# Kernel tuning notes

Measured on AMD Instinct MI355X. Metric: run time of the kernel, lower is better.

Reference implementation:

```python
import jax, jax.numpy as jnp
import numpy as np

NUM_HEADS = 16
THETA = 10000.0


def _rope(x, pos, theta):
    # x: [b, h, s, d_k] with d_k even; rotate interleaved pairs (even, odd)
    d = x.shape[-1]
    inv_freq = theta ** (-jnp.arange(0, d, 2, dtype=jnp.float32) / d)  # [d/2]
    ang = pos.astype(jnp.float32)[:, None] * inv_freq                  # [s, d/2]
    cos = jnp.cos(ang)[None, None]                                     # [1,1,s,d/2]
    sin = jnp.sin(ang)[None, None]
    x1 = x[..., 0::2]
    x2 = x[..., 1::2]
    r1 = x1 * cos - x2 * sin
    r2 = x1 * sin + x2 * cos
    return jnp.stack([r1, r2], axis=-1).reshape(x.shape)


def setup_inputs() -> dict:
    key = jax.random.key(0)
    ks = jax.random.split(key, 5)
    B, S, D = 2, 2048, 1024
    x = jax.random.normal(ks[0], (B, S, D), dtype=jnp.float32)
    scale = 0.02
    Wq = jax.random.normal(ks[1], (D, D), dtype=jnp.float32) * scale
    Wk = jax.random.normal(ks[2], (D, D), dtype=jnp.float32) * scale
    Wv = jax.random.normal(ks[3], (D, D), dtype=jnp.float32) * scale
    Wo = jax.random.normal(ks[4], (D, D), dtype=jnp.float32) * scale
    return {"x": x, "Wq": Wq, "Wk": Wk, "Wv": Wv, "Wo": Wo}


def reference(x, Wq, Wk, Wv, Wo):
    B, S, D = x.shape
    H = NUM_HEADS
    dk = D // H
    # QKV projections (bias-free Linear: y = x @ W^T, W is [out, in])
    q = (x @ Wq.T).reshape(B, S, H, dk).transpose(0, 2, 1, 3)  # [b,h,s,dk]
    k = (x @ Wk.T).reshape(B, S, H, dk).transpose(0, 2, 1, 3)
    v = (x @ Wv.T).reshape(B, S, H, dk).transpose(0, 2, 1, 3)
    pos = jnp.arange(S)
    q = _rope(q, pos, THETA)
    k = _rope(k, pos, THETA)
    # naive masked SDPA, causal mask
    scores = jnp.einsum('bhqd,bhkd->bhqk', q, k) / (dk ** 0.5)
    causal = jnp.tril(jnp.ones((S, S), dtype=bool))
    scores = jnp.where(causal, scores, -jnp.inf)
    attn = jax.nn.softmax(scores, axis=-1)
    out = jnp.einsum('bhqk,bhkd->bhqd', attn, v)
    out = out.transpose(0, 2, 1, 3).reshape(B, S, D)
    return out @ Wo.T
```

## Files before the change

### kernel.cpp

```cpp
#include <hip/hip_runtime.h>
#include <hip/hip_bf16.h>
#include <stdint.h>

typedef __bf16 bf16;
typedef __bf16 bf16x8 __attribute__((ext_vector_type(8)));
typedef float f32x4 __attribute__((ext_vector_type(4)));
typedef float f32x16 __attribute__((ext_vector_type(16)));

#define B_ 2
#define S_ 2048
#define D_ 1024
#define H_ 16
#define DK 64
#define M_ 4096

__device__ __forceinline__ void gload_lds16(const void* g, void* l) {
  __builtin_amdgcn_global_load_lds(
      (const __attribute__((address_space(1))) uint32_t*)(uintptr_t)g,
      (__attribute__((address_space(3))) uint32_t*)(uintptr_t)l, 16, 0, 0);
}

__device__ __forceinline__ uint32_t pkbf(float a, float b) {
  union { uint32_t u; struct { bf16 x, y; } s; } r;
  r.s.x = (bf16)a; r.s.y = (bf16)b;
  return r.u;
}

struct alignas(8) B4s { bf16 a, b, c, d; };

__global__ __launch_bounds__(256) void cvt_all_kernel(
    const float* __restrict__ x, const float* __restrict__ wq, const float* __restrict__ wk,
    const float* __restrict__ wv, const float* __restrict__ wo,
    bf16* __restrict__ xb, bf16* __restrict__ wqb, bf16* __restrict__ wkb,
    bf16* __restrict__ wvb, bf16* __restrict__ wob) {
  int i = blockIdx.x * 256 + threadIdx.x;
  const float* src;
  bf16* dst;
  int off;
  if (i < 1048576) { src = x; dst = xb; off = i; }
  else if (i < 1310720) { src = wq; dst = wqb; off = i - 1048576; }
  else if (i < 1572864) { src = wk; dst = wkb; off = i - 1310720; }
  else if (i < 1835008) { src = wv; dst = wvb; off = i - 1572864; }
  else { src = wo; dst = wob; off = i - 1835008; }
  float4 v = reinterpret_cast<const float4*>(src)[off];
  B4s o{(bf16)v.x, (bf16)v.y, (bf16)v.z, (bf16)v.w};
  reinterpret_cast<B4s*>(dst)[off] = o;
}

template <int MODE>
__global__ __launch_bounds__(256, 3) void gemm_kernel(
    const bf16* __restrict__ A,
    const bf16* __restrict__ W0, const bf16* __restrict__ W1, const bf16* __restrict__ W2,
    bf16* __restrict__ q_out, bf16* __restrict__ k_out, bf16* __restrict__ v_out,
    float* __restrict__ c_out) {
  constexpr int BK = 64;
  constexpr int BM = (MODE == 0) ? 128 : 64;
  constexpr int AM = (MODE == 0) ? 2 : 1;
  constexpr int NT = (MODE == 0) ? 24 : 8;
  constexpr int PERX = (MODE == 0) ? 96 : 64;
  __shared__ bf16 Alds[BM * BK];
  __shared__ bf16 Blds[128 * BK];
  const int tid = threadIdx.x;
  const int w = tid >> 6, l = tid & 63;
  const int l31 = l & 31, hh = l >> 5;
  const int lin = (blockIdx.x & 7) * PERX + (blockIdx.x >> 3);
  const int m0 = (lin / NT) * BM;
  const int nt = lin % NT;
  const bf16* W;
  int n0;
  const int rt = (MODE == 0) ? (nt >> 3) : 0;
  if (MODE == 0) {
    W = rt == 0 ? W0 : (rt == 1 ? W1 : W2);
    n0 = (nt & 7) * 128;
  } else {
    W = W0;
    n0 = nt * 128;
  }
  const int K = 1024;
  const int wm = (MODE == 0) ? (w >> 1) * 64 : (w & 1) * 32;
  const int wn = (MODE == 0) ? (w & 1) * 64 : (w >> 1) * 64;
  const int srow = w * 8 + (l >> 3);
  const int scol = ((l & 7) * 8) ^ (((l >> 3) & 7) * 8);
  const int swz = (l & 7) * 8;
  f32x16 acc[AM][2] = {};
  for (int k0 = 0; k0 < K; k0 += BK) {
    const bf16* Ab = A + (size_t)m0 * K + k0;
    const bf16* Bb = W + (size_t)n0 * K + k0;
#pragma unroll
    for (int c = 0; c < BM / 32; ++c)
      gload_lds16(Ab + (size_t)(c * 32 + srow) * K + scol, Alds + (c * 32 + w * 8) * BK);
#pragma unroll
    for (int c = 0; c < 4; ++c)
      gload_lds16(Bb + (size_t)(c * 32 + srow) * K + scol, Blds + (c * 32 + w * 8) * BK);
    __syncthreads();
    bf16x8 af[AM][4], bfr[2][4];
#pragma unroll
    for (int am = 0; am < AM; ++am)
#pragma unroll
      for (int t = 0; t < 4; ++t)
        af[am][t] = *reinterpret_cast<const bf16x8*>(
            Alds + (wm + am * 32 + l31) * BK + ((t * 16 + hh * 8) ^ swz));
#pragma unroll
    for (int bn = 0; bn < 2; ++bn)
#pragma unroll
      for (int t = 0; t < 4; ++t)
        bfr[bn][t] = *reinterpret_cast<const bf16x8*>(
            Blds + (wn + bn * 32 + l31) * BK + ((t * 16 + hh * 8) ^ swz));
#pragma unroll
    for (int t = 0; t < 4; ++t)
#pragma unroll
      for (int am = 0; am < AM; ++am)
#pragma unroll
        for (int bn = 0; bn < 2; ++bn)
          acc[am][bn] = __builtin_amdgcn_mfma_f32_32x32x16_bf16(af[am][t], bfr[bn][t],
                                                               acc[am][bn], 0, 0, 0);
    __syncthreads();
  }
#pragma unroll
  for (int am = 0; am < AM; ++am)
#pragma unroll
    for (int bn = 0; bn < 2; ++bn)
#pragma unroll
      for (int r = 0; r < 16; ++r) {
        int m = m0 + wm + am * 32 + (r & 3) + 8 * (r >> 2) + 4 * hh;
        int n = n0 + wn + bn * 32 + l31;
        float v = acc[am][bn][r];
        if (MODE == 0) {
          bf16* dst = rt == 0 ? q_out : (rt == 1 ? k_out : v_out);
          int h = n >> 6, d = n & 63;
          int b = m >> 11, s = m & 2047;
          dst[(((size_t)b * H_ + h) * S_ + s) * DK + d] = (bf16)v;
        } else {
          c_out[(size_t)m * D_ + n] = v;
        }
      }
}

__global__ __launch_bounds__(256) void rope_kernel(bf16* __restrict__ Q, bf16* __restrict__ K) {
  const int NG = 32 * 2048 * 8;
  int idx = blockIdx.x * 256 + threadIdx.x;
  bf16* X = Q;
  float sc = 0.18033688f;
  if (idx >= NG) { X = K; idx -= NG; sc = 1.0f; }
  int g = idx & 7;
  int s = (idx >> 3) & 2047;
  int bh = idx >> 14;
  size_t off = ((size_t)bh * S_ + s) * DK + g * 8;
  bf16x8 v = *reinterpret_cast<const bf16x8*>(X + off);
  bf16x8 o;
  const float c0 = -0.4152410118609203f;
  float fs = (float)s;
#pragma unroll
  for (int p = 0; p < 4; ++p) {
    int i = g * 4 + p;
    float ang = fs * exp2f((float)i * c0);
    float sn = __sinf(ang), cs = __cosf(ang);
    float x1 = (float)v[2 * p], x2 = (float)v[2 * p + 1];
    o[2 * p]     = (bf16)((x1 * cs - x2 * sn) * sc);
    o[2 * p + 1] = (bf16)((x1 * sn + x2 * cs) * sc);
  }
  *reinterpret_cast<bf16x8*>(X + off) = o;
}

__global__ __launch_bounds__(256, 4) void attn_kernel(
    const bf16* __restrict__ Q, const bf16* __restrict__ K, const bf16* __restrict__ V,
    bf16* __restrict__ O) {
  __shared__ __align__(16) char smem[40960];
  bf16* K3 = (bf16*)smem;
  bf16* Vt2 = (bf16*)smem + 12288;
  float* MG = (float*)smem;
  const int tid = threadIdx.x;
  const int w = tid >> 6, l = tid & 63;
  const int ql = l & 31, h = l >> 5;
  const int kh = w >> 1, qh = w & 1;
  const int bid = blockIdx.x;
  const int u = (bid >> 5) & 7;
  const int j = bid >> 8;
  const int qt = (j == 0) ? u : (j == 1) ? 31 - u : (j == 2) ? u + 8 : 23 - u;
  const int bh = bid & 31;
  const size_t base = (size_t)bh * S_ * DK;

  const size_t qrow = base + (size_t)(qt * 64 + qh * 32 + ql) * DK;
  bf16x8 qf[4];
#pragma unroll
  for (int t = 0; t < 4; ++t)
    qf[t] = *reinterpret_cast<const bf16x8*>(Q + qrow + t * 16 + h * 8);

  float l_run = 0.f;
  f32x16 o0 = {}, o1 = {};

  auto stageK = [&](int kt, int buf) {
#pragma unroll
    for (int c = 0; c < 2; ++c) {
      int row = c * 32 + w * 8 + (l >> 3);
      int col = ((l & 7) * 8) ^ ((row & 7) * 8);
      gload_lds16(K + base + (size_t)(kt * 64 + row) * DK + col,
                  K3 + buf * 4096 + c * 2048 + w * 512);
    }
  };
  auto loadV = [&](int kt, bf16x8 (&pv)[2]) {
    const bf16* vp = V + base + (size_t)(kt * 64 + l) * DK + w * 16;
    pv[0] = *reinterpret_cast<const bf16x8*>(vp);
    pv[1] = *reinterpret_cast<const bf16x8*>(vp + 8);
  };
  auto writeV = [&](int vb, const bf16x8 (&pv)[2]) {
    bf16* Vt = Vt2 + vb * 4096;
#pragma unroll
    for (int j2 = 0; j2 < 8; ++j2) {
      Vt[(w * 16 + j2) * 64 + (l ^ (j2 * 8))] = pv[0][j2];
      Vt[(w * 16 + 8 + j2) * 64 + (l ^ (j2 * 8))] = pv[1][j2];
    }
  };

  {
    bf16x8 pv[2];
    loadV(0, pv);
    stageK(0, 0);
    if (qt >= 1) stageK(1, 1);
    writeV(0, pv);
    if (qt >= 1) {
      asm volatile("s_waitcnt vmcnt(2)" ::: "memory");
    } else {
      asm volatile("s_waitcnt vmcnt(0)" ::: "memory");
    }
    asm volatile("s_waitcnt lgkmcnt(0)" ::: "memory");
    __builtin_amdgcn_sched_barrier(0);
    __builtin_amdgcn_s_barrier();
    __builtin_amdgcn_sched_barrier(0);
  }

  const int swzd = (ql & 7) * 8;
  const int keyA = kh * 32 + ql;
  const int limq = qh * 32 + ql;
  bf16x8 pvv[2];
  int kb = 0, kb2 = 2;

  for (int kt = 0; kt <= qt; ++kt) {
    const int vb = kt & 1;
    const bool pre = kt < qt;
    const bool pre2 = kt + 2 <= qt;
    const bool lastt = (kt == qt);
    const bool skipw = lastt && (kh == 1) && (qh == 0);
    if (pre) loadV(kt + 1, pvv);
    if (pre2) stageK(kt + 2, kb2);
    if (!skipw) {
      f32x16 ss = {};
      __builtin_amdgcn_s_setprio(1);
#pragma unroll
      for (int t = 0; t < 4; ++t) {
        bf16x8 kf = *reinterpret_cast<const bf16x8*>(
            K3 + kb * 4096 + keyA * 64 + ((t * 16 + h * 8) ^ ((keyA & 7) * 8)));
        ss = __builtin_amdgcn_mfma_f32_32x32x16_bf16(kf, qf[t], ss, 0, 0, 0);
      }
      __builtin_amdgcn_s_setprio(0);
      if (lastt) {
#pragma unroll
        for (int r = 0; r < 16; ++r) {
          int kl = kh * 32 + (r & 3) + 8 * (r >> 2) + 4 * h;
          if (kl > limq) ss[r] = -INFINITY;
        }
      }
      float t0 = 0.f, t1 = 0.f, t2 = 0.f, t3 = 0.f;
#pragma unroll
      for (int r = 0; r < 16; r += 4) {
        float p0 = exp2f(ss[r]);
        float p1 = exp2f(ss[r + 1]);
        float p2 = exp2f(ss[r + 2]);
        float p3 = exp2f(ss[r + 3]);
        ss[r] = p0; ss[r + 1] = p1; ss[r + 2] = p2; ss[r + 3] = p3;
        t0 += p0; t1 += p1; t2 += p2; t3 += p3;
      }
      l_run += (t0 + t1) + (t2 + t3);
      uint32_t Wq_[4][2];
#pragma unroll
      for (int g = 0; g < 4; ++g) {
        Wq_[g][0] = pkbf(ss[4 * g + 0], ss[4 * g + 1]);
        Wq_[g][1] = pkbf(ss[4 * g + 2], ss[4 * g + 3]);
      }
      __builtin_amdgcn_s_setprio(1);
#pragma unroll
      for (int ks = 0; ks < 2; ++ks) {
        uint32_t a0 = Wq_[2 * ks][0], a1 = Wq_[2 * ks][1];
        uint32_t b0 = Wq_[2 * ks + 1][0], b1 = Wq_[2 * ks + 1][1];
        uint32_t sxa0 = (uint32_t)__shfl_xor((int)a0, 32);
        uint32_t sxa1 = (uint32_t)__shfl_xor((int)a1, 32);
        uint32_t sxb0 = (uint32_t)__shfl_xor((int)b0, 32);
        uint32_t sxb1 = (uint32_t)__shfl_xor((int)b1, 32);
        union { uint32_t u[4]; bf16x8 v; } pa;
        pa.u[0] = h ? sxb0 : a0;
        pa.u[1] = h ? sxb1 : a1;
        pa.u[2] = h ? b0 : sxa0;
        pa.u[3] = h ? b1 : sxa1;
        int col = (kh * 32 + ks * 16 + h * 8) ^ swzd;
        const bf16* Vt = Vt2 + vb * 4096;
        bf16x8 v0 = *reinterpret_cast<const bf16x8*>(&Vt[ql * 64 + col]);
        bf16x8 v1 = *reinterpret_cast<const bf16x8*>(&Vt[(32 + ql) * 64 + col]);
        o0 = __builtin_amdgcn_mfma_f32_32x32x16_bf16(pa.v, v0, o0, 0, 0, 0);
        o1 = __builtin_amdgcn_mfma_f32_32x32x16_bf16(pa.v, v1, o1, 0, 0, 0);
      }
      __builtin_amdgcn_s_setprio(0);
    }
    if (pre) writeV(vb ^ 1, pvv);
    asm volatile("s_waitcnt vmcnt(2)" ::: "memory");
    asm volatile("s_waitcnt lgkmcnt(0)" ::: "memory");
    __builtin_amdgcn_sched_barrier(0);
    __builtin_amdgcn_s_barrier();
    __builtin_amdgcn_sched_barrier(0);
    kb = (kb == 2) ? 0 : kb + 1;
    kb2 = (kb2 == 2) ? 0 : kb2 + 1;
  }

  l_run += __shfl_xor(l_run, 32);
  __syncthreads();
  if (kh == 1) {
    int off = (qh * 64 + l) * 33;
    MG[off] = l_run;
#pragma unroll
    for (int r = 0; r < 16; ++r) {
      MG[off + 1 + r] = o0[r];
      MG[off + 17 + r] = o1[r];
    }
  }
  __syncthreads();
  if (kh == 0) {
    int off = (qh * 64 + l) * 33;
    float inv = 1.0f / (l_run + MG[off]);
    const int b = bh >> 4, hd = bh & 15;
#pragma unroll
    for (int r = 0; r < 16; ++r) {
      int rowl = (r & 3) + 8 * (r >> 2) + 4 * h;
      float invr = __shfl(inv, rowl);
      int qr = qt * 64 + qh * 32 + rowl;
      size_t ooff = ((size_t)b * S_ + qr) * D_ + hd * 64;
      O[ooff + ql] = (bf16)((o0[r] + MG[off + 1 + r]) * invr);
      O[ooff + 32 + ql] = (bf16)((o1[r] + MG[off + 17 + r]) * invr);
    }
  }
}

extern "C" void kernel_launch(void* const* d_in, const int* in_sizes, int n_in,
                              void* d_out, int out_size, void* d_ws, size_t ws_size,
                              hipStream_t stream) {
  const float* x  = (const float*)d_in[0];
  const float* Wq = (const float*)d_in[1];
  const float* Wk = (const float*)d_in[2];
  const float* Wv = (const float*)d_in[3];
  const float* Wo = (const float*)d_in[4];
  float* out = (float*)d_out;
  char* ws = (char*)d_ws;

  bf16* xb  = (bf16*)(ws + ((size_t)0 << 20));
  bf16* wqb = (bf16*)(ws + ((size_t)8 << 20));
  bf16* wkb = (bf16*)(ws + ((size_t)10 << 20));
  bf16* wvb = (bf16*)(ws + ((size_t)12 << 20));
  bf16* wob = (bf16*)(ws + ((size_t)14 << 20));
  bf16* Qb  = (bf16*)(ws + ((size_t)16 << 20));
  bf16* Kb  = (bf16*)(ws + ((size_t)24 << 20));
  bf16* Vb  = (bf16*)(ws + ((size_t)32 << 20));
  bf16* Ob  = (bf16*)(ws + ((size_t)40 << 20));

  cvt_all_kernel<<<8192, 256, 0, stream>>>(x, Wq, Wk, Wv, Wo, xb, wqb, wkb, wvb, wob);
  gemm_kernel<0><<<768, 256, 0, stream>>>(xb, wqb, wkb, wvb, Qb, Kb, Vb, nullptr);
  rope_kernel<<<4096, 256, 0, stream>>>(Qb, Kb);
  attn_kernel<<<1024, 256, 0, stream>>>(Qb, Kb, Vb, Ob);
  gemm_kernel<1><<<512, 256, 0, stream>>>(Ob, wob, nullptr, nullptr, nullptr, nullptr,
                                          nullptr, out);
}
```

Measured before the change: 106.3 us.

## Emit V pre-transposed and swizzled from QKV GEMM, stage via async LDS loads

```diff
diff --git a/kernel.cpp b/kernel.cpp
--- a/kernel.cpp
+++ b/kernel.cpp
@@ -51,7 +51,7 @@
 __global__ __launch_bounds__(256, 3) void gemm_kernel(
     const bf16* __restrict__ A,
     const bf16* __restrict__ W0, const bf16* __restrict__ W1, const bf16* __restrict__ W2,
-    bf16* __restrict__ q_out, bf16* __restrict__ k_out, bf16* __restrict__ v_out,
+    bf16* __restrict__ q_out, bf16* __restrict__ k_out, bf16* __restrict__ vt_out,
     float* __restrict__ c_out) {
   constexpr int BK = 64;
   constexpr int BM = (MODE == 0) ? 128 : 64;
@@ -126,10 +126,15 @@
         int n = n0 + wn + bn * 32 + l31;
         float v = acc[am][bn][r];
         if (MODE == 0) {
-          bf16* dst = rt == 0 ? q_out : (rt == 1 ? k_out : v_out);
           int h = n >> 6, d = n & 63;
           int b = m >> 11, s = m & 2047;
-          dst[(((size_t)b * H_ + h) * S_ + s) * DK + d] = (bf16)v;
+          if (rt == 2) {
+            vt_out[(((size_t)(b * H_ + h) * 32 + (s >> 6)) * 64 + d) * 64 +
+                   ((s & 63) ^ ((d & 7) * 8))] = (bf16)v;
+          } else {
+            bf16* dst = rt == 0 ? q_out : k_out;
+            dst[(((size_t)b * H_ + h) * S_ + s) * DK + d] = (bf16)v;
+          }
         } else {
           c_out[(size_t)m * D_ + n] = v;
         }
@@ -163,7 +168,7 @@
 }
 
 __global__ __launch_bounds__(256, 4) void attn_kernel(
-    const bf16* __restrict__ Q, const bf16* __restrict__ K, const bf16* __restrict__ V,
+    const bf16* __restrict__ Q, const bf16* __restrict__ K, const bf16* __restrict__ VtG,
     bf16* __restrict__ O) {
   __shared__ __align__(16) char smem[40960];
   bf16* K3 = (bf16*)smem;
@@ -179,6 +184,7 @@
   const int qt = (j == 0) ? u : (j == 1) ? 31 - u : (j == 2) ? u + 8 : 23 - u;
   const int bh = bid & 31;
   const size_t base = (size_t)bh * S_ * DK;
+  const size_t vtbase = (size_t)bh * 32 * 4096;
 
   const size_t qrow = base + (size_t)(qt * 64 + qh * 32 + ql) * DK;
   bf16x8 qf[4];
@@ -198,27 +204,18 @@
                   K3 + buf * 4096 + c * 2048 + w * 512);
     }
   };
-  auto loadV = [&](int kt, bf16x8 (&pv)[2]) {
-    const bf16* vp = V + base + (size_t)(kt * 64 + l) * DK + w * 16;
-    pv[0] = *reinterpret_cast<const bf16x8*>(vp);
-    pv[1] = *reinterpret_cast<const bf16x8*>(vp + 8);
+  auto stageV = [&](int kt, int buf) {
+#pragma unroll
+    for (int c = 0; c < 2; ++c)
+      gload_lds16(VtG + vtbase + (size_t)kt * 4096 + c * 2048 + tid * 8,
+                  Vt2 + buf * 4096 + c * 2048 + w * 512);
   };
-  auto writeV = [&](int vb, const bf16x8 (&pv)[2]) {
-    bf16* Vt = Vt2 + vb * 4096;
-#pragma unroll
-    for (int j2 = 0; j2 < 8; ++j2) {
-      Vt[(w * 16 + j2) * 64 + (l ^ (j2 * 8))] = pv[0][j2];
-      Vt[(w * 16 + 8 + j2) * 64 + (l ^ (j2 * 8))] = pv[1][j2];
-    }
-  };
 
   {
-    bf16x8 pv[2];
-    loadV(0, pv);
+    stageV(0, 0);
     stageK(0, 0);
-    if (qt >= 1) stageK(1, 1);
-    writeV(0, pv);
     if (qt >= 1) {
+      stageK(1, 1);
       asm volatile("s_waitcnt vmcnt(2)" ::: "memory");
     } else {
       asm volatile("s_waitcnt vmcnt(0)" ::: "memory");
@@ -232,17 +229,16 @@
   const int swzd = (ql & 7) * 8;
   const int keyA = kh * 32 + ql;
   const int limq = qh * 32 + ql;
-  bf16x8 pvv[2];
   int kb = 0, kb2 = 2;
 
   for (int kt = 0; kt <= qt; ++kt) {
     const int vb = kt & 1;
-    const bool pre = kt < qt;
-    const bool pre2 = kt + 2 <= qt;
+    const bool preV = kt + 1 <= qt;
+    const bool preK = kt + 2 <= qt;
     const bool lastt = (kt == qt);
     const bool skipw = lastt && (kh == 1) && (qh == 0);
-    if (pre) loadV(kt + 1, pvv);
-    if (pre2) stageK(kt + 2, kb2);
+    if (preV) stageV(kt + 1, vb ^ 1);
+    if (preK) stageK(kt + 2, kb2);
     if (!skipw) {
       f32x16 ss = {};
       __builtin_amdgcn_s_setprio(1);
@@ -300,8 +296,11 @@
       }
       __builtin_amdgcn_s_setprio(0);
     }
-    if (pre) writeV(vb ^ 1, pvv);
-    asm volatile("s_waitcnt vmcnt(2)" ::: "memory");
+    if (preK) {
+      asm volatile("s_waitcnt vmcnt(2)" ::: "memory");
+    } else {
+      asm volatile("s_waitcnt vmcnt(0)" ::: "memory");
+    }
     asm volatile("s_waitcnt lgkmcnt(0)" ::: "memory");
     __builtin_amdgcn_sched_barrier(0);
     __builtin_amdgcn_s_barrier();
@@ -356,13 +355,13 @@
   bf16* wob = (bf16*)(ws + ((size_t)14 << 20));
   bf16* Qb  = (bf16*)(ws + ((size_t)16 << 20));
   bf16* Kb  = (bf16*)(ws + ((size_t)24 << 20));
-  bf16* Vb  = (bf16*)(ws + ((size_t)32 << 20));
+  bf16* VtG = (bf16*)(ws + ((size_t)32 << 20));
   bf16* Ob  = (bf16*)(ws + ((size_t)40 << 20));
 
   cvt_all_kernel<<<8192, 256, 0, stream>>>(x, Wq, Wk, Wv, Wo, xb, wqb, wkb, wvb, wob);
-  gemm_kernel<0><<<768, 256, 0, stream>>>(xb, wqb, wkb, wvb, Qb, Kb, Vb, nullptr);
+  gemm_kernel<0><<<768, 256, 0, stream>>>(xb, wqb, wkb, wvb, Qb, Kb, VtG, nullptr);
   rope_kernel<<<4096, 256, 0, stream>>>(Qb, Kb);
-  attn_kernel<<<1024, 256, 0, stream>>>(Qb, Kb, Vb, Ob);
+  attn_kernel<<<1024, 256, 0, stream>>>(Qb, Kb, VtG, Ob);
   gemm_kernel<1><<<512, 256, 0, stream>>>(Ob, wob, nullptr, nullptr, nullptr, nullptr,
                                           nullptr, out);
 }
```

After: 113.4 us. 6.6% more time.
